# Performance work log

Hardware: AMD Instinct MI355X
Metric: run time of the kernel (lower is better)

## Reference

```python
import jax, jax.numpy as jnp
import numpy as np


def sage_conv(x, src, dst, n, W_l, b_l, W_r):
    # PyG SAGEConv (mean aggr): out = lin_l(mean_{j in N(i)} x_j) + lin_r(x_i)
    msg = x[src]                                            # [E, d_in] gather
    s = jax.ops.segment_sum(msg, dst, num_segments=n)       # [N, d_in]
    cnt = jax.ops.segment_sum(jnp.ones((src.shape[0], 1), x.dtype), dst, num_segments=n)
    mean = s / jnp.maximum(cnt, 1.0)
    return mean @ W_l.T + b_l + x @ W_r.T


def setup_inputs() -> dict:
    key = jax.random.key(0)
    ks = jax.random.split(key, 12)
    N, E, D = 200000, 6400000, 128
    x = jax.random.normal(ks[0], (N, D), dtype=jnp.float32)
    edge_index = jax.random.randint(ks[1], (2, E), 0, N, dtype=jnp.int64)

    def lin(k, dout, din, scale=None):
        s = scale if scale is not None else 1.0 / np.sqrt(din)
        return jax.random.uniform(k, (dout, din), jnp.float32, -s, s)

    return {
        "x": x,
        "edge_index": edge_index,
        "W1_l": lin(ks[2], 64, D), "b1_l": jnp.zeros((64,), jnp.float32), "W1_r": lin(ks[3], 64, D),
        "W2_l": lin(ks[4], 32, 64), "b2_l": jnp.zeros((32,), jnp.float32), "W2_r": lin(ks[5], 32, 64),
        "W3_l": lin(ks[6], 16, 32), "b3_l": jnp.zeros((16,), jnp.float32), "W3_r": lin(ks[7], 16, 32),
        "W_reg": lin(ks[8], 1, 16), "b_reg": jnp.zeros((1,), jnp.float32),
        "W_cls": lin(ks[9], 1, 16), "b_cls": jnp.zeros((1,), jnp.float32),
    }


def reference(x, edge_index, W1_l, b1_l, W1_r, W2_l, b2_l, W2_r, W3_l, b3_l, W3_r,
              W_reg, b_reg, W_cls, b_cls):
    # eval mode: dropout is identity
    n = x.shape[0]
    src, dst = edge_index[0], edge_index[1]
    h = jax.nn.relu(sage_conv(x, src, dst, n, W1_l, b1_l, W1_r))
    h = jax.nn.relu(sage_conv(h, src, dst, n, W2_l, b2_l, W2_r))
    h = jax.nn.relu(sage_conv(h, src, dst, n, W3_l, b3_l, W3_r))
    reg = (h @ W_reg.T + b_reg)[:, 0]
    cls = (h @ W_cls.T + b_cls)[:, 0]
    return (reg, cls)
```

## Files before the change

### kernel.cpp

```cpp
#include <hip/hip_runtime.h>


typedef __bf16 bf16x8 __attribute__((ext_vector_type(8)));
typedef float  f32x4  __attribute__((ext_vector_type(4)));

__device__ __forceinline__ unsigned short f2bf_rne(float f) {
    unsigned int u = __float_as_uint(f);
    u = (u + 0x7FFFu + ((u >> 16) & 1u)) >> 16;
    return (unsigned short)u;
}

__device__ __forceinline__ void bfacc(float4& a, const uint2 q) {
    a.x += __uint_as_float(q.x << 16);
    a.y += __uint_as_float(q.x & 0xFFFF0000u);
    a.z += __uint_as_float(q.y << 16);
    a.w += __uint_as_float(q.y & 0xFFFF0000u);
}


__global__ __launch_bounds__(256) void k_bcount(const int* __restrict__ dst, int E, int N,
                                                int* __restrict__ bcnt) {
    __shared__ int h[256];
    const int tid = threadIdx.x;
    h[tid] = 0;
    __syncthreads();
    const int stride = gridDim.x * 256;
    for (int i = blockIdx.x * 256 + tid; i < E; i += stride) {
        int d = dst[i];
        d = d < 0 ? 0 : (d >= N ? N - 1 : d);
        atomicAdd(&h[d >> 10], 1);
    }
    __syncthreads();
    if (h[tid]) atomicAdd(&bcnt[tid], h[tid]);
}

__global__ __launch_bounds__(256) void k_bscan(const int* __restrict__ bcnt,
                                               int* __restrict__ boff, int NBK, int E) {
    __shared__ int sd[256];
    const int tid = threadIdx.x;
    int v = (tid < NBK) ? bcnt[tid] : 0;
    sd[tid] = v; __syncthreads();
    for (int off = 1; off < 256; off <<= 1) {
        int t = (tid >= off) ? sd[tid - off] : 0;
        __syncthreads();
        sd[tid] += t;
        __syncthreads();
    }
    if (tid < NBK) boff[tid] = sd[tid] - v;
    if (tid == 0) boff[NBK] = E;
}

#define BTILE 4096
__global__ __launch_bounds__(256) void k_bucket(const int* __restrict__ src,
                                                const int* __restrict__ dst, int E, int N,
                                                const int* __restrict__ boff,
                                                int* __restrict__ bcur,
                                                int2* __restrict__ T, int NBK) {
    __shared__ int cnt[256], cnt2[256], lofs[256], gbase[256], boffs[256], sd[256];
    __shared__ int2 staged[BTILE];
    const int tid = threadIdx.x;
    const int tb = blockIdx.x * BTILE;
    const int tn = min(BTILE, E - tb);
    cnt[tid] = 0; cnt2[tid] = 0;
    boffs[tid] = (tid < NBK) ? boff[tid] : 0;
    __syncthreads();
    for (int i = tid; i < tn; i += 256) {
        int d = dst[tb + i];
        d = d < 0 ? 0 : (d >= N ? N - 1 : d);
        atomicAdd(&cnt[d >> 10], 1);
    }
    __syncthreads();
    int v = cnt[tid];
    sd[tid] = v; __syncthreads();
    for (int off = 1; off < 256; off <<= 1) {
        int t = (tid >= off) ? sd[tid - off] : 0;
        __syncthreads();
        sd[tid] += t;
        __syncthreads();
    }
    lofs[tid] = sd[tid] - v;
    if (v > 0 && tid < NBK) gbase[tid] = atomicAdd(&bcur[tid], v);
    __syncthreads();
    for (int i = tid; i < tn; i += 256) {
        int d = dst[tb + i];
        d = d < 0 ? 0 : (d >= N ? N - 1 : d);
        int s = src[tb + i];
        s = s < 0 ? 0 : (s >= N ? N - 1 : s);
        int b = d >> 10;
        int r = atomicAdd(&cnt2[b], 1);
        staged[lofs[b] + r] = make_int2(s, d);
    }
    __syncthreads();
    for (int i = tid; i < tn; i += 256) {
        int2 p = staged[i];
        int b = p.y >> 10;
        T[(size_t)boffs[b] + gbase[b] + (i - lofs[b])] = p;
    }
}

__global__ __launch_bounds__(1024) void k_csr(const int2* __restrict__ T,
                                              const int* __restrict__ boff,
                                              int* __restrict__ rowptr,
                                              int* __restrict__ adj, int N, int E) {
    __shared__ int hist[1024];
    __shared__ int sc[1024];
    const int tid = threadIdx.x;
    const int b = blockIdx.x;
    const int node0 = b << 10;
    hist[tid] = 0;
    __syncthreads();
    const int beg = boff[b], end = boff[b + 1];
    for (int i = beg + tid; i < end; i += 1024)
        atomicAdd(&hist[T[i].y - node0], 1);
    __syncthreads();
    int v = hist[tid];
    sc[tid] = v;
    __syncthreads();
    for (int off = 1; off < 1024; off <<= 1) {
        int t = (tid >= off) ? sc[tid - off] : 0;
        __syncthreads();
        sc[tid] += t;
        __syncthreads();
    }
    const int excl = beg + sc[tid] - v;
    const int n = node0 + tid;
    if (n < N) rowptr[n] = excl;
    if (b == 0 && tid == 0) rowptr[N] = E;
    hist[tid] = excl;
    __syncthreads();
    for (int i = beg + tid; i < end; i += 1024) {
        int2 p = T[i];
        int pos = atomicAdd(&hist[p.y - node0], 1);
        adj[pos] = p.x;
    }
}

template<int DIN, int DOUT>
__global__ __launch_bounds__(256) void proj_mfma(const float* __restrict__ H,
                                                 const float* __restrict__ Wl,
                                                 const float* __restrict__ Wr,
                                                 const float* __restrict__ bias,
                                                 unsigned short* __restrict__ Pl,
                                                 float* __restrict__ R, int N) {
    constexpr int SP = DIN + 8;
    constexpr int COLT = DOUT / 16;
    __shared__ __bf16 lwl[DOUT * SP];
    __shared__ __bf16 lwrh[DOUT * SP];
    __shared__ __bf16 lwrl[DOUT * SP];
    for (int idx = threadIdx.x; idx < DIN * DOUT; idx += 256) {
        int c = idx / DIN, k = idx % DIN;
        float wl = Wl[idx], wr = Wr[idx];
        __bf16 wrh = (__bf16)wr;
        lwl[c * SP + k] = (__bf16)wl;
        lwrh[c * SP + k] = wrh;
        lwrl[c * SP + k] = (__bf16)(wr - (float)wrh);
    }
    __syncthreads();
    const int wave = threadIdx.x >> 6, lane = threadIdx.x & 63;
    const int quad = lane >> 4, l16 = lane & 15;
    const int n0 = (blockIdx.x * 4 + wave) * 16;
    int arow = n0 + l16;
    if (arow >= N) arow = N - 1;
    const float* hrow = H + (size_t)arow * DIN;

    f32x4 zero = {0.f, 0.f, 0.f, 0.f};
    f32x4 accP[COLT], accR[COLT];
    #pragma unroll
    for (int t = 0; t < COLT; ++t) { accP[t] = zero; accR[t] = zero; }

    for (int k0 = 0; k0 < DIN; k0 += 32) {
        const float* hp = hrow + k0 + quad * 8;
        float4 h0 = *(const float4*)hp;
        float4 h1 = *(const float4*)(hp + 4);
        float hv[8] = {h0.x, h0.y, h0.z, h0.w, h1.x, h1.y, h1.z, h1.w};
        bf16x8 ahi, alo;
        #pragma unroll
        for (int j = 0; j < 8; ++j) {
            __bf16 hb = (__bf16)hv[j];
            ahi[j] = hb;
            alo[j] = (__bf16)(hv[j] - (float)hb);
        }
        const int kk = k0 + quad * 8;
        #pragma unroll
        for (int t = 0; t < COLT; ++t) {
            const int c = t * 16 + l16;
            bf16x8 bl  = *(const bf16x8*)&lwl [c * SP + kk];
            bf16x8 brh = *(const bf16x8*)&lwrh[c * SP + kk];
            bf16x8 brl = *(const bf16x8*)&lwrl[c * SP + kk];
            accP[t] = __builtin_amdgcn_mfma_f32_16x16x32_bf16(ahi, bl,  accP[t], 0, 0, 0);
            accR[t] = __builtin_amdgcn_mfma_f32_16x16x32_bf16(ahi, brh, accR[t], 0, 0, 0);
            accR[t] = __builtin_amdgcn_mfma_f32_16x16x32_bf16(ahi, brl, accR[t], 0, 0, 0);
            accR[t] = __builtin_amdgcn_mfma_f32_16x16x32_bf16(alo, brh, accR[t], 0, 0, 0);
        }
    }
    #pragma unroll
    for (int t = 0; t < COLT; ++t) {
        const int c = t * 16 + l16;
        const float bc = bias[c];
        #pragma unroll
        for (int r = 0; r < 4; ++r) {
            int node = n0 + quad * 4 + r;
            if (node < N) {
                Pl[(size_t)node * DOUT + c] = f2bf_rne(accP[t][r]);
                R[(size_t)node * DOUT + c] = accR[t][r] + bc;
            }
        }
    }
}


template<int DOUT> struct GatherCfg {
    static constexpr int L   = DOUT / 4;
    static constexpr int S   = 64 / L;
    static constexpr int M   = 4;
    static constexpr int NPW = S * M;
    static constexpr int NPB = NPW * 4;
};

template<int DOUT>
__global__ __launch_bounds__(256, 6) void gather_kernel(const unsigned short* __restrict__ P,
                                                        const int* __restrict__ rowptr,
                                                        const int* __restrict__ adj,
                                                        float* __restrict__ Hout, int N) {
    using C = GatherCfg<DOUT>;
    constexpr int L = C::L, S = C::S, M = C::M;
    constexpr int NPW = C::NPW, NPB = C::NPB;
    const int wave = threadIdx.x >> 6, lane = threadIdx.x & 63;
    const int sub = lane / L, cl = lane % L;
    const uint2* __restrict__ P2 = (const uint2*)P;
    float4* __restrict__ H4 = (float4*)Hout;
    const int base = blockIdx.x * NPB + wave * NPW + sub;
    #pragma unroll 1
    for (int m = 0; m < M; ++m) {
        int n = base + m * S;
        if (n >= N) continue;
        int beg = rowptr[n], end = rowptr[n + 1];
        float4 a0 = {0, 0, 0, 0}, a1 = {0, 0, 0, 0}, a2 = {0, 0, 0, 0}, a3 = {0, 0, 0, 0};
        int j = beg;
        while (j < end && (j & 3)) { bfacc(a0, P2[(size_t)adj[j] * L + cl]); ++j; }
        for (; j + 8 <= end; j += 8) {
            int4 sA = *(const int4*)(adj + j);
            int4 sB = *(const int4*)(adj + j + 4);
            uint2 p0 = P2[(size_t)sA.x * L + cl];
            uint2 p1 = P2[(size_t)sA.y * L + cl];
            uint2 p2 = P2[(size_t)sA.z * L + cl];
            uint2 p3 = P2[(size_t)sA.w * L + cl];
            uint2 p4 = P2[(size_t)sB.x * L + cl];
            uint2 p5 = P2[(size_t)sB.y * L + cl];
            uint2 p6 = P2[(size_t)sB.z * L + cl];
            uint2 p7 = P2[(size_t)sB.w * L + cl];
            bfacc(a0, p0); bfacc(a1, p1); bfacc(a2, p2); bfacc(a3, p3);
            bfacc(a0, p4); bfacc(a1, p5); bfacc(a2, p6); bfacc(a3, p7);
        }
        if (j + 4 <= end) {
            int4 sA = *(const int4*)(adj + j);
            bfacc(a0, P2[(size_t)sA.x * L + cl]);
            bfacc(a1, P2[(size_t)sA.y * L + cl]);
            bfacc(a2, P2[(size_t)sA.z * L + cl]);
            bfacc(a3, P2[(size_t)sA.w * L + cl]);
            j += 4;
        }
        for (; j < end; ++j) bfacc(a0, P2[(size_t)adj[j] * L + cl]);
        int deg = end - beg;
        float inv = deg > 0 ? 1.0f / (float)deg : 0.0f;
        float4 r = H4[(size_t)n * L + cl];
        float4 o;
        o.x = fmaxf((a0.x + a1.x + a2.x + a3.x) * inv + r.x, 0.0f);
        o.y = fmaxf((a0.y + a1.y + a2.y + a3.y) * inv + r.y, 0.0f);
        o.z = fmaxf((a0.z + a1.z + a2.z + a3.z) * inv + r.z, 0.0f);
        o.w = fmaxf((a0.w + a1.w + a2.w + a3.w) * inv + r.w, 0.0f);
        H4[(size_t)n * L + cl] = o;
    }
}

__global__ __launch_bounds__(256) void k_head(const float* __restrict__ H3,
                                              const float* __restrict__ Wreg,
                                              const float* __restrict__ breg,
                                              const float* __restrict__ Wcls,
                                              const float* __restrict__ bcls,
                                              float* __restrict__ out, int N) {
    int i = blockIdx.x * 256 + threadIdx.x;
    if (i >= N) return;
    const float4* h = (const float4*)(H3 + (size_t)i * 16);
    float reg = 0.f, cls = 0.f;
    #pragma unroll
    for (int k4 = 0; k4 < 4; ++k4) {
        float4 hv = h[k4];
        float4 wr = ((const float4*)Wreg)[k4];
        float4 wc = ((const float4*)Wcls)[k4];
        reg += hv.x * wr.x + hv.y * wr.y + hv.z * wr.z + hv.w * wr.w;
        cls += hv.x * wc.x + hv.y * wc.y + hv.z * wc.z + hv.w * wc.w;
    }
    out[i] = reg + breg[0];
    out[(size_t)N + i] = cls + bcls[0];
}

extern "C" void kernel_launch(void* const* d_in, const int* in_sizes, int n_in,
                              void* d_out, int out_size, void* d_ws, size_t ws_size,
                              hipStream_t stream) {
    const float* x    = (const float*)d_in[0];
    const int*   ei   = (const int*)d_in[1];
    const float* W1l  = (const float*)d_in[2];
    const float* b1l  = (const float*)d_in[3];
    const float* W1r  = (const float*)d_in[4];
    const float* W2l  = (const float*)d_in[5];
    const float* b2l  = (const float*)d_in[6];
    const float* W2r  = (const float*)d_in[7];
    const float* W3l  = (const float*)d_in[8];
    const float* b3l  = (const float*)d_in[9];
    const float* W3r  = (const float*)d_in[10];
    const float* Wreg = (const float*)d_in[11];
    const float* breg = (const float*)d_in[12];
    const float* Wcls = (const float*)d_in[13];
    const float* bcls = (const float*)d_in[14];

    const int N = in_sizes[0] / 128;
    const int E = in_sizes[1] / 2;
    const int* src = ei;
    const int* dst = ei + E;

    char* ws = (char*)d_ws;
    size_t off = 0;
    auto alloc = [&](size_t bytes) -> void* {
        void* p = ws + off;
        off += (bytes + 255) & ~(size_t)255;
        return p;
    };
    int*   rowptr = (int*)alloc((size_t)(N + 1) * 4);
    int*   bcnt   = (int*)alloc(1024);
    int*   bcur   = (int*)alloc(1024);
    int*   boff   = (int*)alloc(1028);
    int*   adj    = (int*)alloc((size_t)E * 4);
    unsigned short* A = (unsigned short*)alloc((size_t)N * 64 * 2);
    float* B      = (float*)alloc((size_t)N * 64 * 4);
    float* C      = (float*)alloc((size_t)N * 32 * 4);
    float* D      = (float*)alloc((size_t)N * 16 * 4);
    int2*  T      = (int2*)B;

    const int NBK = (N + 1023) >> 10;

    hipMemsetAsync(bcnt, 0, 1024, stream);
    hipMemsetAsync(bcur, 0, 1024, stream);
    k_bcount<<<1024, 256, 0, stream>>>(dst, E, N, bcnt);
    k_bscan<<<1, 256, 0, stream>>>(bcnt, boff, NBK, E);
    k_bucket<<<(E + BTILE - 1) / BTILE, 256, 0, stream>>>(src, dst, E, N, boff, bcur, T, NBK);
    k_csr<<<NBK, 1024, 0, stream>>>(T, boff, rowptr, adj, N, E);

    const int PB = 64;
    constexpr int G64 = GatherCfg<64>::NPB;
    constexpr int G32 = GatherCfg<32>::NPB;
    constexpr int G16 = GatherCfg<16>::NPB;

    proj_mfma<128, 64><<<(N + PB - 1) / PB, 256, 0, stream>>>(x, W1l, W1r, b1l, A, B, N);
    gather_kernel<64><<<(N + G64 - 1) / G64, 256, 0, stream>>>(A, rowptr, adj, B, N);
    proj_mfma<64, 32><<<(N + PB - 1) / PB, 256, 0, stream>>>(B, W2l, W2r, b2l, A, C, N);
    gather_kernel<32><<<(N + G32 - 1) / G32, 256, 0, stream>>>(A, rowptr, adj, C, N);
    proj_mfma<32, 16><<<(N + PB - 1) / PB, 256, 0, stream>>>(C, W3l, W3r, b3l, A, D, N);
    gather_kernel<16><<<(N + G16 - 1) / G16, 256, 0, stream>>>(A, rowptr, adj, D, N);

    k_head<<<(N + 255) / 256, 256, 0, stream>>>(D, Wreg, breg, Wcls, bcls, (float*)d_out, N);
}
```

Measured before the change: 745.7 us.

## Pack bucketed edges into one int, widen gather loads to 16 bytes

The bucketed edge array now stores each edge as a single 32-bit word: the 10-bit local destination sits in the high bits and the 18-bit source in the low bits. This halves the write and read traffic of the bucket and CSR-build passes, and it relies on N being at most 2^18. The gather kernels now load 8 bf16 features per lane with uint4 loads, so each lane covers twice as many channels and there are half as many load instructions. The bcur memset is folded into the scan kernel to drop one launch. The wider lanes halve the lanes per node and change how many nodes each wave covers, which may shift latency hiding and occupancy.

```diff
diff --git a/kernel.cpp b/kernel.cpp
--- a/kernel.cpp
+++ b/kernel.cpp
@@ -10,11 +10,15 @@
     return (unsigned short)u;
 }
 
-__device__ __forceinline__ void bfacc(float4& a, const uint2 q) {
-    a.x += __uint_as_float(q.x << 16);
-    a.y += __uint_as_float(q.x & 0xFFFF0000u);
-    a.z += __uint_as_float(q.y << 16);
-    a.w += __uint_as_float(q.y & 0xFFFF0000u);
+__device__ __forceinline__ void bfacc8(float4& lo, float4& hi, const uint4 q) {
+    lo.x += __uint_as_float(q.x << 16);
+    lo.y += __uint_as_float(q.x & 0xFFFF0000u);
+    lo.z += __uint_as_float(q.y << 16);
+    lo.w += __uint_as_float(q.y & 0xFFFF0000u);
+    hi.x += __uint_as_float(q.z << 16);
+    hi.y += __uint_as_float(q.z & 0xFFFF0000u);
+    hi.z += __uint_as_float(q.w << 16);
+    hi.w += __uint_as_float(q.w & 0xFFFF0000u);
 }
 
 
@@ -35,9 +39,11 @@
 }
 
 __global__ __launch_bounds__(256) void k_bscan(const int* __restrict__ bcnt,
-                                               int* __restrict__ boff, int NBK, int E) {
+                                               int* __restrict__ boff,
+                                               int* __restrict__ bcur, int NBK, int E) {
     __shared__ int sd[256];
     const int tid = threadIdx.x;
+    bcur[tid] = 0;
     int v = (tid < NBK) ? bcnt[tid] : 0;
     sd[tid] = v; __syncthreads();
     for (int off = 1; off < 256; off <<= 1) {
@@ -55,7 +61,7 @@
                                                 const int* __restrict__ dst, int E, int N,
                                                 const int* __restrict__ boff,
                                                 int* __restrict__ bcur,
-                                                int2* __restrict__ T, int NBK) {
+                                                int* __restrict__ T, int NBK) {
     __shared__ int cnt[256], cnt2[256], lofs[256], gbase[256], boffs[256], sd[256];
     __shared__ int2 staged[BTILE];
     const int tid = threadIdx.x;
@@ -94,11 +100,11 @@
     for (int i = tid; i < tn; i += 256) {
         int2 p = staged[i];
         int b = p.y >> 10;
-        T[(size_t)boffs[b] + gbase[b] + (i - lofs[b])] = p;
-    }
-}
-
-__global__ __launch_bounds__(1024) void k_csr(const int2* __restrict__ T,
+        T[(size_t)boffs[b] + gbase[b] + (i - lofs[b])] = ((p.y & 1023) << 18) | p.x;
+    }
+}
+
+__global__ __launch_bounds__(1024) void k_csr(const int* __restrict__ T,
                                               const int* __restrict__ boff,
                                               int* __restrict__ rowptr,
                                               int* __restrict__ adj, int N, int E) {
@@ -111,7 +117,7 @@
     __syncthreads();
     const int beg = boff[b], end = boff[b + 1];
     for (int i = beg + tid; i < end; i += 1024)
-        atomicAdd(&hist[T[i].y - node0], 1);
+        atomicAdd(&hist[((unsigned)T[i]) >> 18], 1);
     __syncthreads();
     int v = hist[tid];
     sc[tid] = v;
@@ -129,9 +135,9 @@
     hist[tid] = excl;
     __syncthreads();
     for (int i = beg + tid; i < end; i += 1024) {
-        int2 p = T[i];
-        int pos = atomicAdd(&hist[p.y - node0], 1);
-        adj[pos] = p.x;
+        unsigned p = (unsigned)T[i];
+        int pos = atomicAdd(&hist[p >> 18], 1);
+        adj[pos] = (int)(p & 0x3FFFFu);
     }
 }
 
@@ -210,7 +216,7 @@
 
 
 template<int DOUT> struct GatherCfg {
-    static constexpr int L   = DOUT / 4;
+    static constexpr int L   = DOUT / 8;
     static constexpr int S   = 64 / L;
     static constexpr int M   = 4;
     static constexpr int NPW = S * M;
@@ -227,7 +233,7 @@
     constexpr int NPW = C::NPW, NPB = C::NPB;
     const int wave = threadIdx.x >> 6, lane = threadIdx.x & 63;
     const int sub = lane / L, cl = lane % L;
-    const uint2* __restrict__ P2 = (const uint2*)P;
+    const uint4* __restrict__ P4 = (const uint4*)P;
     float4* __restrict__ H4 = (float4*)Hout;
     const int base = blockIdx.x * NPB + wave * NPW + sub;
     #pragma unroll 1
@@ -235,41 +241,49 @@
         int n = base + m * S;
         if (n >= N) continue;
         int beg = rowptr[n], end = rowptr[n + 1];
-        float4 a0 = {0, 0, 0, 0}, a1 = {0, 0, 0, 0}, a2 = {0, 0, 0, 0}, a3 = {0, 0, 0, 0};
+        float4 a0l = {0,0,0,0}, a0h = {0,0,0,0}, a1l = {0,0,0,0}, a1h = {0,0,0,0};
         int j = beg;
-        while (j < end && (j & 3)) { bfacc(a0, P2[(size_t)adj[j] * L + cl]); ++j; }
+        while (j < end && (j & 3)) { bfacc8(a0l, a0h, P4[(size_t)adj[j] * L + cl]); ++j; }
         for (; j + 8 <= end; j += 8) {
             int4 sA = *(const int4*)(adj + j);
             int4 sB = *(const int4*)(adj + j + 4);
-            uint2 p0 = P2[(size_t)sA.x * L + cl];
-            uint2 p1 = P2[(size_t)sA.y * L + cl];
-            uint2 p2 = P2[(size_t)sA.z * L + cl];
-            uint2 p3 = P2[(size_t)sA.w * L + cl];
-            uint2 p4 = P2[(size_t)sB.x * L + cl];
-            uint2 p5 = P2[(size_t)sB.y * L + cl];
-            uint2 p6 = P2[(size_t)sB.z * L + cl];
-            uint2 p7 = P2[(size_t)sB.w * L + cl];
-            bfacc(a0, p0); bfacc(a1, p1); bfacc(a2, p2); bfacc(a3, p3);
-            bfacc(a0, p4); bfacc(a1, p5); bfacc(a2, p6); bfacc(a3, p7);
+            uint4 q0 = P4[(size_t)sA.x * L + cl];
+            uint4 q1 = P4[(size_t)sA.y * L + cl];
+            uint4 q2 = P4[(size_t)sA.z * L + cl];
+            uint4 q3 = P4[(size_t)sA.w * L + cl];
+            uint4 q4 = P4[(size_t)sB.x * L + cl];
+            uint4 q5 = P4[(size_t)sB.y * L + cl];
+            uint4 q6 = P4[(size_t)sB.z * L + cl];
+            uint4 q7 = P4[(size_t)sB.w * L + cl];
+            bfacc8(a0l, a0h, q0); bfacc8(a1l, a1h, q1);
+            bfacc8(a0l, a0h, q2); bfacc8(a1l, a1h, q3);
+            bfacc8(a0l, a0h, q4); bfacc8(a1l, a1h, q5);
+            bfacc8(a0l, a0h, q6); bfacc8(a1l, a1h, q7);
         }
         if (j + 4 <= end) {
             int4 sA = *(const int4*)(adj + j);
-            bfacc(a0, P2[(size_t)sA.x * L + cl]);
-            bfacc(a1, P2[(size_t)sA.y * L + cl]);
-            bfacc(a2, P2[(size_t)sA.z * L + cl]);
-            bfacc(a3, P2[(size_t)sA.w * L + cl]);
+            bfacc8(a0l, a0h, P4[(size_t)sA.x * L + cl]);
+            bfacc8(a1l, a1h, P4[(size_t)sA.y * L + cl]);
+            bfacc8(a0l, a0h, P4[(size_t)sA.z * L + cl]);
+            bfacc8(a1l, a1h, P4[(size_t)sA.w * L + cl]);
             j += 4;
         }
-        for (; j < end; ++j) bfacc(a0, P2[(size_t)adj[j] * L + cl]);
+        for (; j < end; ++j) bfacc8(a0l, a0h, P4[(size_t)adj[j] * L + cl]);
         int deg = end - beg;
         float inv = deg > 0 ? 1.0f / (float)deg : 0.0f;
-        float4 r = H4[(size_t)n * L + cl];
-        float4 o;
-        o.x = fmaxf((a0.x + a1.x + a2.x + a3.x) * inv + r.x, 0.0f);
-        o.y = fmaxf((a0.y + a1.y + a2.y + a3.y) * inv + r.y, 0.0f);
-        o.z = fmaxf((a0.z + a1.z + a2.z + a3.z) * inv + r.z, 0.0f);
-        o.w = fmaxf((a0.w + a1.w + a2.w + a3.w) * inv + r.w, 0.0f);
-        H4[(size_t)n * L + cl] = o;
+        float4 rlo = H4[(size_t)n * L * 2 + cl * 2];
+        float4 rhi = H4[(size_t)n * L * 2 + cl * 2 + 1];
+        float4 olo, ohi;
+        olo.x = fmaxf((a0l.x + a1l.x) * inv + rlo.x, 0.0f);
+        olo.y = fmaxf((a0l.y + a1l.y) * inv + rlo.y, 0.0f);
+        olo.z = fmaxf((a0l.z + a1l.z) * inv + rlo.z, 0.0f);
+        olo.w = fmaxf((a0l.w + a1l.w) * inv + rlo.w, 0.0f);
+        ohi.x = fmaxf((a0h.x + a1h.x) * inv + rhi.x, 0.0f);
+        ohi.y = fmaxf((a0h.y + a1h.y) * inv + rhi.y, 0.0f);
+        ohi.z = fmaxf((a0h.z + a1h.z) * inv + rhi.z, 0.0f);
+        ohi.w = fmaxf((a0h.w + a1h.w) * inv + rhi.w, 0.0f);
+        H4[(size_t)n * L * 2 + cl * 2]     = olo;
+        H4[(size_t)n * L * 2 + cl * 2 + 1] = ohi;
     }
 }
 
@@ -335,14 +349,13 @@
     float* B      = (float*)alloc((size_t)N * 64 * 4);
     float* C      = (float*)alloc((size_t)N * 32 * 4);
     float* D      = (float*)alloc((size_t)N * 16 * 4);
-    int2*  T      = (int2*)B;
+    int*   T      = (int*)B;
 
     const int NBK = (N + 1023) >> 10;
 
     hipMemsetAsync(bcnt, 0, 1024, stream);
-    hipMemsetAsync(bcur, 0, 1024, stream);
     k_bcount<<<1024, 256, 0, stream>>>(dst, E, N, bcnt);
-    k_bscan<<<1, 256, 0, stream>>>(bcnt, boff, NBK, E);
+    k_bscan<<<1, 256, 0, stream>>>(bcnt, boff, bcur, NBK, E);
     k_bucket<<<(E + BTILE - 1) / BTILE, 256, 0, stream>>>(src, dst, E, N, boff, bcur, T, NBK);
     k_csr<<<NBK, 1024, 0, stream>>>(T, boff, rowptr, adj, N, E);
 
```

Result: slower. 794.0 us (+6.5%).
